# Kernel optimization log

Measured on AMD Instinct MI355X. Metric: run time of the kernel, lower is better.

## Reference

```python
import jax, jax.numpy as jnp
import numpy as np

HID = 128          # hidden_dim
IN_DIM = 256       # input_dim
BOT = 128          # bottleneck_dim
OUT = 4            # output_dim
NQ = 131072        # num query (mesh) points
E = 262144         # num grid->query edges
SEQ = 262144       # grid points (64^3)
B = 1
PE_DIM = 4 * HID   # 512, sincos embed dim over ndim=4


def _linear_params(key, fin, fout):
    k1, k2 = jax.random.split(key)
    lim = 1.0 / np.sqrt(fin)
    w = jax.random.uniform(k1, (fin, fout), minval=-lim, maxval=lim, dtype=jnp.float32)
    b = jax.random.uniform(k2, (fout,), minval=-lim, maxval=lim, dtype=jnp.float32)
    return w, b


def setup_inputs() -> dict:
    key = jax.random.key(0)
    ks = jax.random.split(key, 10)
    x = jax.random.normal(ks[0], (B, SEQ, IN_DIM), dtype=jnp.float32)
    # raw positions in [0, 200) so query_pos/100 - 1 lands in [-1, 1)
    query_pos = jax.random.uniform(ks[1], (NQ, 3), dtype=jnp.float32) * 200.0
    qidx = jnp.sort(jax.random.randint(ks[2], (E,), 0, NQ))          # sorted, as segment_csr assumes
    gidx = jax.random.randint(ks[3], (E,), 0, B * SEQ)
    grid_to_query_edges = jnp.stack([qidx, gidx], axis=1)            # [E, 2] (query_idx, grid_idx)

    msg_w0, msg_b0 = _linear_params(ks[4], IN_DIM + PE_DIM, 512)
    msg_w1, msg_b1 = _linear_params(ks[5], 512, 256)
    msg_w2, msg_b2 = _linear_params(ks[6], 256, BOT)
    pred_w0, pred_b0 = _linear_params(ks[7], BOT, 256)
    pred_w1, pred_b1 = _linear_params(ks[8], 256, OUT)
    return dict(x=x, query_pos=query_pos, grid_to_query_edges=grid_to_query_edges,
                msg_w0=msg_w0, msg_b0=msg_b0, msg_w1=msg_w1, msg_b1=msg_b1,
                msg_w2=msg_w2, msg_b2=msg_b2,
                pred_w0=pred_w0, pred_b0=pred_b0, pred_w1=pred_w1, pred_b1=pred_b1)


def _sincos_embed(coords):
    # coords: [N, 4]; dim=512 -> 128 per coord -> 64 frequencies (no padding needed)
    eff = PE_DIM // 4
    omega = 1.0 / (10000.0 ** (jnp.arange(0, eff, 2, dtype=jnp.float32) / eff))  # [64]
    out = coords[..., None] * omega                                  # [N, 4, 64]
    emb = jnp.concatenate([jnp.sin(out), jnp.cos(out)], axis=-1)     # [N, 4, 128]
    return emb.reshape(coords.shape[0], -1)                          # [N, 512]


def _gelu(x):
    return jax.nn.gelu(x, approximate=False)  # torch nn.GELU default is exact erf


def reference(x, query_pos, grid_to_query_edges,
              msg_w0, msg_b0, msg_w1, msg_b1, msg_w2, msg_b2,
              pred_w0, pred_b0, pred_w1, pred_b1):
    qp = query_pos / 100.0 - 1.0
    ones = jnp.ones((qp.shape[0], 1), dtype=qp.dtype)
    qp = jnp.concatenate([qp, ones], axis=1)                         # [NQ, 4]
    pe = _sincos_embed(qp)                                           # [NQ, 512]

    xf = x.reshape(-1, x.shape[-1])                                  # [B*SEQ, IN_DIM]
    qidx = grid_to_query_edges[:, 0]
    gidx = grid_to_query_edges[:, 1]

    feat = jnp.concatenate([xf[gidx], pe[qidx]], axis=1)             # [E, 768]
    h = _gelu(feat @ msg_w0 + msg_b0)
    h = _gelu(h @ msg_w1 + msg_b1)
    h = h @ msg_w2 + msg_b2                                          # [E, BOT]

    nq = qp.shape[0]
    sums = jax.ops.segment_sum(h, qidx, num_segments=nq)             # [NQ, BOT]
    counts = jax.ops.segment_sum(jnp.ones((h.shape[0],), h.dtype), qidx, num_segments=nq)
    mean = sums / jnp.maximum(counts, 1.0)[:, None]                  # empty segments -> 0 (segment_csr mean)

    out = _gelu(mean @ pred_w0 + pred_b0) @ pred_w1 + pred_b1        # [NQ, OUT]
    return out
```

## Files before the change

### kernel.cpp

```cpp
#include <hip/hip_runtime.h>
#include <cmath>

#define IN_DIM   256
#define H0_DIM   512
#define H1_DIM   256
#define BOT      128
#define NQ_      131072
#define NE_      262144
#define SEQ_     262144
#define QWIN     32768
#define NWIN     (NQ_/QWIN)
#define PE_K     384

static const size_t OFF_XH    = 0;
static const size_t OFF_XL    = 134217728;
static const size_t OFF_Z     = 268435456;
static const size_t OFF_PEH   = 536870912;
static const size_t OFF_PEL   = 562036736;
static const size_t OFF_H2    = 738197504;
static const size_t OFF_W0AH  = 872415232;
static const size_t OFF_W0AL  = 872677376;
static const size_t OFF_W0BH  = 872939520;
static const size_t OFF_W0BL  = 873332736;
static const size_t OFF_W1H   = 873725952;
static const size_t OFF_W1L   = 873988096;
static const size_t OFF_W2H   = 874250240;
static const size_t OFF_W2L   = 874315776;
static const size_t OFF_PW0H  = 874381312;
static const size_t OFF_PW0L  = 874446848;
static const size_t OFF_BCONST= 874512384;
static const size_t OFF_START = 874514432;
static const size_t OFF_MEANH = 0;
static const size_t OFF_MEANL = 33554432;
static const size_t OFF_G1    = 268435456;

typedef __attribute__((ext_vector_type(8))) short bf16x8;
typedef __attribute__((ext_vector_type(4))) float f32x4;

__device__ __forceinline__ float gelu_f(float v) {
    return v * 0.5f * (1.0f + erff(v * 0.7071067811865476f));
}
__device__ __forceinline__ unsigned short f2bf(float f) {
    unsigned int u = __float_as_uint(f);
    unsigned int r = (u + 0x7FFFu + ((u >> 16) & 1u)) >> 16;
    return (unsigned short)r;
}
__device__ __forceinline__ float bf2f(unsigned short h) {
    return __uint_as_float(((unsigned int)h) << 16);
}
__device__ __forceinline__ unsigned int pack2(unsigned short a, unsigned short b) {
    return (unsigned int)a | ((unsigned int)b << 16);
}
__device__ __forceinline__ void stage16(const void* g, void* l) {
    __builtin_amdgcn_global_load_lds(
        (const __attribute__((address_space(1))) unsigned int*)g,
        (__attribute__((address_space(3))) unsigned int*)l,
        16, 0, 0);
}
#define WAITV0 asm volatile("s_waitcnt vmcnt(0)" ::: "memory")
#define WAITV6 asm volatile("s_waitcnt vmcnt(6)" ::: "memory")
#define WAITV8 asm volatile("s_waitcnt vmcnt(8)" ::: "memory")
#define WAITL0 asm volatile("s_waitcnt lgkmcnt(0)" ::: "memory")

__device__ __forceinline__ void cvt4(const float4 v, unsigned int* hw, unsigned int* lw) {
    const unsigned short a = f2bf(v.x), b = f2bf(v.y), c = f2bf(v.z), d = f2bf(v.w);
    hw[0] = pack2(a, b); hw[1] = pack2(c, d);
    lw[0] = pack2(f2bf(v.x - bf2f(a)), f2bf(v.y - bf2f(b)));
    lw[1] = pack2(f2bf(v.z - bf2f(c)), f2bf(v.w - bf2f(d)));
}

__global__ __launch_bounds__(256) void conv_x(
    const float* __restrict__ x,
    unsigned short* __restrict__ xH, unsigned short* __restrict__ xL)
{
    const int wv = threadIdx.x >> 6;
    const int l  = threadIdx.x & 63;
    const int row = blockIdx.x * 4 + wv;
    const size_t base = (size_t)row * IN_DIM + l * 4;
    float4 v = *(const float4*)&x[base];
    unsigned short h0 = f2bf(v.x), h1 = f2bf(v.y), h2 = f2bf(v.z), h3 = f2bf(v.w);
    uint2 H, L;
    H.x = pack2(h0, h1); H.y = pack2(h2, h3);
    L.x = pack2(f2bf(v.x - bf2f(h0)), f2bf(v.y - bf2f(h1)));
    L.y = pack2(f2bf(v.z - bf2f(h2)), f2bf(v.w - bf2f(h3)));
    *(uint2*)&xH[base] = H;
    *(uint2*)&xL[base] = L;
}

__global__ __launch_bounds__(256) void conv_w(
    const float* __restrict__ W, unsigned short* __restrict__ WTh,
    unsigned short* __restrict__ WTl, int K, int N)
{
    int idx = blockIdx.x * 256 + threadIdx.x;
    if (idx >= K * N) return;
    int k = idx / N, n = idx % N;
    float v = W[idx];
    unsigned short h = f2bf(v);
    WTh[(size_t)n * K + k] = h;
    WTl[(size_t)n * K + k] = f2bf(v - bf2f(h));
}

__global__ __launch_bounds__(256) void bias_fold(
    const float* __restrict__ w0, const float* __restrict__ b0,
    float* __restrict__ bconst)
{
    int n = blockIdx.x * 256 + threadIdx.x;
    if (n >= H0_DIM) return;
    float s = b0[n];
    for (int j = 0; j < 64; ++j) {
        float om = exp2f((float)j * (-13.287712379549449f / 64.0f));
        s += sinf(om) * w0[(size_t)(640 + j) * H0_DIM + n];
        s += cosf(om) * w0[(size_t)(704 + j) * H0_DIM + n];
    }
    bconst[n] = s;
}

__global__ __launch_bounds__(256) void seg_offsets(
    const int* __restrict__ edges, int* __restrict__ start)
{
    int e = blockIdx.x * 256 + threadIdx.x;
    if (e > NE_) return;
    int qc = (e < NE_) ? edges[2 * e] : NQ_;
    int qp = (e > 0) ? edges[2 * e - 2] : -1;
    for (int q = qp + 1; q <= qc; ++q) start[q] = e;
}

__global__ __launch_bounds__(256) void build_pe(
    const float* __restrict__ qpos, int qbase,
    unsigned short* __restrict__ peH, unsigned short* __restrict__ peL)
{
    const int wv = threadIdx.x >> 6;
    const int l  = threadIdx.x & 63;
    const int i  = blockIdx.x * 4 + wv;
    const int i0 = l * 8;
    if (i0 >= PE_K) return;
    const int q  = qbase + i;
    const size_t base = (size_t)i * PE_K;

    const int cc = i0 >> 7;
    const int j0 = i0 & 127;
    const float cv = qpos[q * 3 + cc] * 0.01f - 1.0f;
    const bool is_sin = (j0 < 64);
    const int jj0 = j0 & 63;
    unsigned int hw[4], lw[4];
    #pragma unroll
    for (int p2 = 0; p2 < 4; ++p2) {
        unsigned short hh[2], ll[2];
        #pragma unroll
        for (int s = 0; s < 2; ++s) {
            int jj = jj0 + p2 * 2 + s;
            float om  = exp2f((float)jj * (-13.287712379549449f / 64.0f));
            float arg = cv * om;
            float v   = is_sin ? __sinf(arg) : __cosf(arg);
            unsigned short h = f2bf(v);
            hh[s] = h; ll[s] = f2bf(v - bf2f(h));
        }
        hw[p2] = pack2(hh[0], hh[1]);
        lw[p2] = pack2(ll[0], ll[1]);
    }
    uint4 H, L;
    H.x = hw[0]; H.y = hw[1]; H.z = hw[2]; H.w = hw[3];
    L.x = lw[0]; L.y = lw[1]; L.z = lw[2]; L.w = lw[3];
    *(uint4*)&peH[base + i0] = H;
    *(uint4*)&peL[base + i0] = L;
}

template <int ACT, int OUT_MODE, int GATHER>
__global__ __launch_bounds__(256) void gemm_mfma(
    const unsigned short* __restrict__ Ah, const unsigned short* __restrict__ Al,
    const unsigned short* __restrict__ Bh, const unsigned short* __restrict__ Bl,
    const float* __restrict__ bias,
    float* __restrict__ Cf, unsigned short* __restrict__ ChO, unsigned short* __restrict__ ClO,
    int M, int K, int N,
    const int* __restrict__ gp, const float* __restrict__ Zw)
{
    __shared__ __align__(16) short lds[2][4][128][32];

    const int tid = threadIdx.x;
    const int w   = tid >> 6;
    const int l   = tid & 63;
    const int l16 = l & 15;
    const int lq  = l >> 4;
    const int bm  = blockIdx.y * 128;
    const int bn  = blockIdx.x * 128;
    const int wm  = (w & 1) * 64;
    const int wn  = (w >> 1) * 64;

    f32x4 acc[4][4];
    #pragma unroll
    for (int i = 0; i < 4; ++i)
        #pragma unroll
        for (int j = 0; j < 4; ++j)
            acc[i][j] = (f32x4){0.f, 0.f, 0.f, 0.f};

    const int jrow = l >> 2;
    const int jkc  = l & 3;
    const int jswz = (jkc ^ (jrow & 3)) * 8;
    const int rswz = (lq ^ (l16 & 3)) * 8;
    const int t0 = w * 2, t1 = t0 + 1;
    const int r0 = t0 * 16 + jrow, r1 = t1 * 16 + jrow;

    size_t arow0, arow1;
    if (GATHER) {
        arow0 = (size_t)gp[2 * (bm + r0) + 1] * K;
        arow1 = (size_t)gp[2 * (bm + r1) + 1] * K;
    } else {
        arow0 = (size_t)(bm + r0) * K;
        arow1 = (size_t)(bm + r1) * K;
    }
    const size_t brow0 = (size_t)(bn + r0) * K;
    const size_t brow1 = (size_t)(bn + r1) * K;

    const int NK = K >> 5;

    auto stage_set = [&](int k, int cb) {
        const int ko = (k << 5) + jswz;
        short* base = &lds[cb][0][0][0];
        stage16(Ah + arow0 + ko, base + t0 * 512);
        stage16(Al + arow0 + ko, base + 4096 + t0 * 512);
        stage16(Bh + brow0 + ko, base + 8192 + t0 * 512);
        stage16(Bl + brow0 + ko, base + 12288 + t0 * 512);
        stage16(Ah + arow1 + ko, base + t1 * 512);
        stage16(Al + arow1 + ko, base + 4096 + t1 * 512);
        stage16(Bh + brow1 + ko, base + 8192 + t1 * 512);
        stage16(Bl + brow1 + ko, base + 12288 + t1 * 512);
    };

    stage_set(0, 0);
    if (NK > 1) stage_set(1, 1);

    for (int ks = 0; ks < NK; ++ks) {
        const int cur = ks & 1;
        if (ks == NK - 1) { WAITV0; } else { WAITV8; }
        __builtin_amdgcn_s_barrier();

        bf16x8 ah[4], al[4], bh[4], bl[4];
        #pragma unroll
        for (int i = 0; i < 4; ++i) {
            ah[i] = *(const bf16x8*)&lds[cur][0][wm + i*16 + l16][rswz];
            al[i] = *(const bf16x8*)&lds[cur][1][wm + i*16 + l16][rswz];
            bh[i] = *(const bf16x8*)&lds[cur][2][wn + i*16 + l16][rswz];
            bl[i] = *(const bf16x8*)&lds[cur][3][wn + i*16 + l16][rswz];
        }
        WAITL0;
        __builtin_amdgcn_sched_barrier(0);
        __builtin_amdgcn_s_barrier();
        if (ks + 2 < NK) stage_set(ks + 2, cur);

        #pragma unroll
        for (int i = 0; i < 4; ++i)
            #pragma unroll
            for (int j = 0; j < 4; ++j) {
                acc[i][j] = __builtin_amdgcn_mfma_f32_16x16x32_bf16(ah[i], bh[j], acc[i][j], 0, 0, 0);
                acc[i][j] = __builtin_amdgcn_mfma_f32_16x16x32_bf16(ah[i], bl[j], acc[i][j], 0, 0, 0);
                acc[i][j] = __builtin_amdgcn_mfma_f32_16x16x32_bf16(al[i], bh[j], acc[i][j], 0, 0, 0);
            }
    }

    if (OUT_MODE == 0) {
        #pragma unroll
        for (int j = 0; j < 4; ++j) {
            int n = bn + wn + j * 16 + l16;
            float bv = bias[n];
            #pragma unroll
            for (int i = 0; i < 4; ++i) {
                int mrow = bm + wm + i * 16 + lq * 4;
                #pragma unroll
                for (int r = 0; r < 4; ++r) {
                    float v = acc[i][j][r] + bv;
                    if (ACT) v = gelu_f(v);
                    Cf[(size_t)(mrow + r) * N + n] = v;
                }
            }
        }
    }
}

__global__ __launch_bounds__(256, 2) void fused_edge(
    const unsigned short* __restrict__ xHg, const unsigned short* __restrict__ xLg,
    const unsigned short* __restrict__ w0aHg, const unsigned short* __restrict__ w0aLg,
    const unsigned short* __restrict__ w1Hg, const unsigned short* __restrict__ w1Lg,
    const unsigned short* __restrict__ w2Hg, const unsigned short* __restrict__ w2Lg,
    const float* __restrict__ Zg, const float* __restrict__ b1g,
    const float* __restrict__ b2g, const int* __restrict__ gp,
    float* __restrict__ h2g)
{
    extern __shared__ __align__(16) short smem[];
    short* h0h = smem + 24576;
    short* h0l = smem + 32768;

    const int tid = threadIdx.x;
    const int w   = tid >> 6;
    const int l   = tid & 63;
    const int l16 = l & 15;
    const int lq  = l >> 4;
    const int bm  = blockIdx.x * 64;

    const int wn_p = w * 32;
    const int wn1  = w * 64;

    const int rx = tid >> 2;
    const int ux = tid & 3;
    const int sx = (ux ^ (rx & 3)) * 8;
    const int rswz = (lq ^ (l16 & 3)) * 8;
    const size_t xoff = (size_t)gp[2 * (bm + rx) + 1] * IN_DIM + sx;
    const int q_e = gp[2 * (bm + l)];
    float* lbuf = ((float*)smem) + w * 2048;

    f32x4 h1acc[4][4];
    #pragma unroll
    for (int i = 0; i < 4; ++i)
        #pragma unroll
        for (int j = 0; j < 4; ++j)
            h1acc[i][j] = (f32x4){0.f, 0.f, 0.f, 0.f};

    for (int c = 0; c < 4; ++c) {
        f32x4 acc1[4][2];
        #pragma unroll
        for (int i = 0; i < 4; ++i)
            #pragma unroll
            for (int j = 0; j < 2; ++j)
                acc1[i][j] = (f32x4){0.f, 0.f, 0.f, 0.f};

        auto stage1 = [&](int k, short* B) {
            const int ko = k << 5;
            const size_t wo = (size_t)(c * 128 + rx) * IN_DIM + ko + sx;
            stage16(xHg + xoff + ko, B + tid * 8);
            stage16(xLg + xoff + ko, B + 2048 + tid * 8);
            stage16(w0aHg + wo,                       B + 4096 + tid * 8);
            stage16(w0aHg + wo + (size_t)64 * IN_DIM, B + 6144 + tid * 8);
            stage16(w0aLg + wo,                       B + 8192 + tid * 8);
            stage16(w0aLg + wo + (size_t)64 * IN_DIM, B + 10240 + tid * 8);
        };

        stage1(0, smem);
        stage1(1, smem + 12288);
        for (int ks = 0; ks < 8; ++ks) {
            short* B = (ks & 1) ? (smem + 12288) : smem;
            if (ks == 7) { WAITV0; } else { WAITV6; }
            __builtin_amdgcn_s_barrier();

            bf16x8 ah[4], al[4], bh[2], bl[2];
            #pragma unroll
            for (int i = 0; i < 4; ++i) {
                const int ro = (i * 16 + l16) * 32 + rswz;
                ah[i] = *(const bf16x8*)&B[ro];
                al[i] = *(const bf16x8*)&B[2048 + ro];
            }
            #pragma unroll
            for (int j = 0; j < 2; ++j) {
                const int ro = (wn_p + j * 16 + l16) * 32 + rswz;
                bh[j] = *(const bf16x8*)&B[4096 + ro];
                bl[j] = *(const bf16x8*)&B[8192 + ro];
            }
            WAITL0;
            __builtin_amdgcn_sched_barrier(0);
            __builtin_amdgcn_s_barrier();
            if (ks < 6) stage1(ks + 2, B);

            #pragma unroll
            for (int i = 0; i < 4; ++i)
                #pragma unroll
                for (int j = 0; j < 2; ++j) {
                    acc1[i][j] = __builtin_amdgcn_mfma_f32_16x16x32_bf16(ah[i], bh[j], acc1[i][j], 0, 0, 0);
                    acc1[i][j] = __builtin_amdgcn_mfma_f32_16x16x32_bf16(ah[i], bl[j], acc1[i][j], 0, 0, 0);
                    acc1[i][j] = __builtin_amdgcn_mfma_f32_16x16x32_bf16(al[i], bh[j], acc1[i][j], 0, 0, 0);
                }
        }
        __syncthreads();

        #pragma unroll
        for (int j = 0; j < 2; ++j)
            #pragma unroll
            for (int i = 0; i < 4; ++i)
                #pragma unroll
                for (int r = 0; r < 4; ++r) {
                    const int rowq = i * 16 + lq * 4 + r;
                    const int u = j * 4 + (l16 >> 2);
                    lbuf[rowq * 32 + (((u ^ (rowq & 7)) << 2) | (l16 & 3))] = acc1[i][j][r];
                }
        __syncthreads();
        {
            const float* zrow = Zg + (size_t)q_e * H0_DIM + c * 128 + wn_p;
            #pragma unroll
            for (int g = 0; g < 2; ++g) {
                unsigned int hw[8], lw[8];
                #pragma unroll
                for (int c2 = 0; c2 < 4; ++c2) {
                    const int cq = g * 4 + c2;
                    float4 v = *(const float4*)&lbuf[l * 32 + ((cq ^ (l & 7)) << 2)];
                    const float4 z = *(const float4*)&zrow[cq * 4];
                    v.x = gelu_f(v.x + z.x); v.y = gelu_f(v.y + z.y);
                    v.z = gelu_f(v.z + z.z); v.w = gelu_f(v.w + z.w);
                    cvt4(v, &hw[c2 * 2], &lw[c2 * 2]);
                }
                const int u0 = (wn_p >> 3) + g * 2;
                const int o0 = l * 128 + (((u0    ) ^ (l & 7)) << 3);
                const int o1 = l * 128 + (((u0 + 1) ^ (l & 7)) << 3);
                uint4 H0, H1, L0, L1;
                H0.x = hw[0]; H0.y = hw[1]; H0.z = hw[2]; H0.w = hw[3];
                H1.x = hw[4]; H1.y = hw[5]; H1.z = hw[6]; H1.w = hw[7];
                L0.x = lw[0]; L0.y = lw[1]; L0.z = lw[2]; L0.w = lw[3];
                L1.x = lw[4]; L1.y = lw[5]; L1.z = lw[6]; L1.w = lw[7];
                *(uint4*)&h0h[o0] = H0; *(uint4*)&h0h[o1] = H1;
                *(uint4*)&h0l[o0] = L0; *(uint4*)&h0l[o1] = L1;
            }
        }
        __syncthreads();

        {
            #pragma unroll
            for (int p = 0; p < 4; ++p) {
                const size_t o = (size_t)(rx + 64 * p) * H0_DIM + c * 128 + sx;
                stage16(w1Hg + o, smem + p * 2048 + tid * 8);
                stage16(w1Lg + o, smem + 8192 + p * 2048 + tid * 8);
            }
        }
        __syncthreads();
        for (int ks = 0; ks < 4; ++ks) {
            bf16x8 ah[4], al[4], bh[4], bl[4];
            #pragma unroll
            for (int i = 0; i < 4; ++i) {
                const int row = i * 16 + l16;
                const int uo = ((ks * 4 + lq) ^ (row & 7)) << 3;
                ah[i] = *(const bf16x8*)&h0h[row * 128 + uo];
                al[i] = *(const bf16x8*)&h0l[row * 128 + uo];
            }
            #pragma unroll
            for (int j = 0; j < 4; ++j) {
                const int ro = (wn1 + j * 16 + l16) * 32 + rswz;
                bh[j] = *(const bf16x8*)&smem[ro];
                bl[j] = *(const bf16x8*)&smem[8192 + ro];
            }
            __syncthreads();
            if (ks < 3) {
                #pragma unroll
                for (int p = 0; p < 4; ++p) {
                    const size_t o = (size_t)(rx + 64 * p) * H0_DIM + c * 128 + (ks + 1) * 32 + sx;
                    stage16(w1Hg + o, smem + p * 2048 + tid * 8);
                    stage16(w1Lg + o, smem + 8192 + p * 2048 + tid * 8);
                }
            }
            #pragma unroll
            for (int i = 0; i < 4; ++i)
                #pragma unroll
                for (int j = 0; j < 4; ++j) {
                    h1acc[i][j] = __builtin_amdgcn_mfma_f32_16x16x32_bf16(ah[i], bh[j], h1acc[i][j], 0, 0, 0);
                    h1acc[i][j] = __builtin_amdgcn_mfma_f32_16x16x32_bf16(ah[i], bl[j], h1acc[i][j], 0, 0, 0);
                    h1acc[i][j] = __builtin_amdgcn_mfma_f32_16x16x32_bf16(al[i], bh[j], h1acc[i][j], 0, 0, 0);
                }
            __syncthreads();
        }
    }

    f32x4 acc2[4][2];
    #pragma unroll
    for (int i = 0; i < 4; ++i)
        #pragma unroll
        for (int j = 0; j < 2; ++j)
            acc2[i][j] = (f32x4){0.f, 0.f, 0.f, 0.f};

    for (int kh = 0; kh < 2; ++kh) {
        const bool my = ((w >> 1) == kh);
        #pragma unroll
        for (int j2 = 0; j2 < 2; ++j2) {
            if (my) {
                #pragma unroll
                for (int jj = 0; jj < 2; ++jj) {
                    const int j = j2 * 2 + jj;
                    const float bv = b1g[wn1 + j * 16 + l16];
                    #pragma unroll
                    for (int i = 0; i < 4; ++i)
                        #pragma unroll
                        for (int r = 0; r < 4; ++r) {
                            const int rowq = i * 16 + lq * 4 + r;
                            const int u = jj * 4 + (l16 >> 2);
                            lbuf[rowq * 32 + (((u ^ (rowq & 7)) << 2) | (l16 & 3))] =
                                gelu_f(h1acc[i][j][r] + bv);
                        }
                }
            }
            __syncthreads();
            if (my) {
                const int colb = (w & 1) * 64 + j2 * 32;
                #pragma unroll
                for (int g = 0; g < 2; ++g) {
                    unsigned int hw[8], lw[8];
                    #pragma unroll
                    for (int c2 = 0; c2 < 4; ++c2) {
                        const int cq = g * 4 + c2;
                        float4 v = *(const float4*)&lbuf[l * 32 + ((cq ^ (l & 7)) << 2)];
                        cvt4(v, &hw[c2 * 2], &lw[c2 * 2]);
                    }
                    const int u0 = ((colb + g * 16) >> 3);
                    const int o0 = l * 128 + (((u0    ) ^ (l & 7)) << 3);
                    const int o1 = l * 128 + (((u0 + 1) ^ (l & 7)) << 3);
                    uint4 H0, H1, L0, L1;
                    H0.x = hw[0]; H0.y = hw[1]; H0.z = hw[2]; H0.w = hw[3];
                    H1.x = hw[4]; H1.y = hw[5]; H1.z = hw[6]; H1.w = hw[7];
                    L0.x = lw[0]; L0.y = lw[1]; L0.z = lw[2]; L0.w = lw[3];
                    L1.x = lw[4]; L1.y = lw[5]; L1.z = lw[6]; L1.w = lw[7];
                    *(uint4*)&h0h[o0] = H0; *(uint4*)&h0h[o1] = H1;
                    *(uint4*)&h0l[o0] = L0; *(uint4*)&h0l[o1] = L1;
                }
            }
            __syncthreads();
        }

        {
            #pragma unroll
            for (int p = 0; p < 2; ++p) {
                const size_t o = (size_t)(rx + 64 * p) * H1_DIM + kh * 128 + sx;
                stage16(w2Hg + o, smem + p * 2048 + tid * 8);
                stage16(w2Lg + o, smem + 4096 + p * 2048 + tid * 8);
            }
        }
        __syncthreads();
        for (int ks = 0; ks < 4; ++ks) {
            bf16x8 ah[4], al[4], bh[2], bl[2];
            #pragma unroll
            for (int i = 0; i < 4; ++i) {
                const int row = i * 16 + l16;
                const int uo = ((ks * 4 + lq) ^ (row & 7)) << 3;
                ah[i] = *(const bf16x8*)&h0h[row * 128 + uo];
                al[i] = *(const bf16x8*)&h0l[row * 128 + uo];
            }
            #pragma unroll
            for (int j = 0; j < 2; ++j) {
                const int ro = (wn_p + j * 16 + l16) * 32 + rswz;
                bh[j] = *(const bf16x8*)&smem[ro];
                bl[j] = *(const bf16x8*)&smem[4096 + ro];
            }
            __syncthreads();
            if (ks < 3) {
                #pragma unroll
                for (int p = 0; p < 2; ++p) {
                    const size_t o = (size_t)(rx + 64 * p) * H1_DIM + kh * 128 + (ks + 1) * 32 + sx;
                    stage16(w2Hg + o, smem + p * 2048 + tid * 8);
                    stage16(w2Lg + o, smem + 4096 + p * 2048 + tid * 8);
                }
            }
            #pragma unroll
            for (int i = 0; i < 4; ++i)
                #pragma unroll
                for (int j = 0; j < 2; ++j) {
                    acc2[i][j] = __builtin_amdgcn_mfma_f32_16x16x32_bf16(ah[i], bh[j], acc2[i][j], 0, 0, 0);
                    acc2[i][j] = __builtin_amdgcn_mfma_f32_16x16x32_bf16(ah[i], bl[j], acc2[i][j], 0, 0, 0);
                    acc2[i][j] = __builtin_amdgcn_mfma_f32_16x16x32_bf16(al[i], bh[j], acc2[i][j], 0, 0, 0);
                }
            __syncthreads();
        }
    }

    #pragma unroll
    for (int j = 0; j < 2; ++j) {
        const int n = wn_p + j * 16 + l16;
        const float bv = b2g[n];
        #pragma unroll
        for (int i = 0; i < 4; ++i) {
            const int er = bm + i * 16 + lq * 4;
            #pragma unroll
            for (int r = 0; r < 4; ++r)
                h2g[(size_t)(er + r) * BOT + n] = acc2[i][j][r] + bv;
        }
    }
}

__global__ __launch_bounds__(256) void seg_mean(
    const int* __restrict__ start, const float* __restrict__ h2,
    unsigned short* __restrict__ mH, unsigned short* __restrict__ mL)
{
    const int t = threadIdx.x;
    const int q = blockIdx.x * 8 + (t >> 5);
    const int quad = t & 31;
    const int s = start[q];
    const int e = start[q + 1];

    float4 acc = make_float4(0.f, 0.f, 0.f, 0.f);
    for (int i = s; i < e; ++i) {
        const float4 v = *(const float4*)&h2[(size_t)i * BOT + quad * 4];
        acc.x += v.x; acc.y += v.y; acc.z += v.z; acc.w += v.w;
    }
    const float inv = 1.0f / (float)((e - s) > 0 ? (e - s) : 1);
    float m0 = acc.x * inv, m1 = acc.y * inv, m2 = acc.z * inv, m3 = acc.w * inv;
    unsigned short h0 = f2bf(m0), h1 = f2bf(m1), h2s = f2bf(m2), h3 = f2bf(m3);
    uint2 H, L;
    H.x = pack2(h0, h1); H.y = pack2(h2s, h3);
    L.x = pack2(f2bf(m0 - bf2f(h0)), f2bf(m1 - bf2f(h1)));
    L.y = pack2(f2bf(m2 - bf2f(h2s)), f2bf(m3 - bf2f(h3)));
    *(uint2*)&mH[(size_t)q * BOT + quad * 4] = H;
    *(uint2*)&mL[(size_t)q * BOT + quad * 4] = L;
}

__global__ __launch_bounds__(256) void pred1_kernel(
    const float* __restrict__ g1, const float* __restrict__ w,
    const float* __restrict__ b, float* __restrict__ out)
{
    const int wave = threadIdx.x >> 6;
    const int lane = threadIdx.x & 63;
    const int row  = blockIdx.x * 4 + wave;

    const float* g = g1 + (size_t)row * 256;
    float a0 = 0, a1 = 0, a2 = 0, a3 = 0;
    #pragma unroll
    for (int i = 0; i < 4; ++i) {
        int k = lane + 64 * i;
        float gv = g[k];
        const float* wr = w + k * 4;
        a0 = fmaf(gv, wr[0], a0);
        a1 = fmaf(gv, wr[1], a1);
        a2 = fmaf(gv, wr[2], a2);
        a3 = fmaf(gv, wr[3], a3);
    }
    #pragma unroll
    for (int off = 32; off > 0; off >>= 1) {
        a0 += __shfl_down(a0, off, 64);
        a1 += __shfl_down(a1, off, 64);
        a2 += __shfl_down(a2, off, 64);
        a3 += __shfl_down(a3, off, 64);
    }
    if (lane == 0) {
        float4 o = {a0 + b[0], a1 + b[1], a2 + b[2], a3 + b[3]};
        *(float4*)&out[(size_t)row * 4] = o;
    }
}

extern "C" void kernel_launch(void* const* d_in, const int* in_sizes, int n_in,
                              void* d_out, int out_size, void* d_ws, size_t ws_size,
                              hipStream_t stream)
{
    const float* x    = (const float*)d_in[0];
    const float* qpos = (const float*)d_in[1];
    const int*   edges= (const int*)  d_in[2];
    const float* w0   = (const float*)d_in[3];
    const float* b0   = (const float*)d_in[4];
    const float* w1   = (const float*)d_in[5];
    const float* b1   = (const float*)d_in[6];
    const float* w2   = (const float*)d_in[7];
    const float* b2   = (const float*)d_in[8];
    const float* pw0  = (const float*)d_in[9];
    const float* pb0  = (const float*)d_in[10];
    const float* pw1  = (const float*)d_in[11];
    const float* pb1  = (const float*)d_in[12];
    float* out = (float*)d_out;

    char* ws = (char*)d_ws;
    unsigned short* xH    = (unsigned short*)(ws + OFF_XH);
    unsigned short* xL    = (unsigned short*)(ws + OFF_XL);
    float*          Z     = (float*)(ws + OFF_Z);
    unsigned short* peH   = (unsigned short*)(ws + OFF_PEH);
    unsigned short* peL   = (unsigned short*)(ws + OFF_PEL);
    float*          h2    = (float*)(ws + OFF_H2);
    unsigned short* w0aH  = (unsigned short*)(ws + OFF_W0AH);
    unsigned short* w0aL  = (unsigned short*)(ws + OFF_W0AL);
    unsigned short* w0bH  = (unsigned short*)(ws + OFF_W0BH);
    unsigned short* w0bL  = (unsigned short*)(ws + OFF_W0BL);
    unsigned short* w1H   = (unsigned short*)(ws + OFF_W1H);
    unsigned short* w1L   = (unsigned short*)(ws + OFF_W1L);
    unsigned short* w2H   = (unsigned short*)(ws + OFF_W2H);
    unsigned short* w2L   = (unsigned short*)(ws + OFF_W2L);
    unsigned short* pw0H  = (unsigned short*)(ws + OFF_PW0H);
    unsigned short* pw0L  = (unsigned short*)(ws + OFF_PW0L);
    float*          bconst= (float*)(ws + OFF_BCONST);
    int*            start = (int*)(ws + OFF_START);
    unsigned short* meanH = (unsigned short*)(ws + OFF_MEANH);
    unsigned short* meanL = (unsigned short*)(ws + OFF_MEANL);
    float*          g1    = (float*)(ws + OFF_G1);

    static bool attr_done = false;
    if (!attr_done) {
        hipFuncSetAttribute(reinterpret_cast<const void*>(&fused_edge),
                            hipFuncAttributeMaxDynamicSharedMemorySize, 81920);
        attr_done = true;
    }

    conv_x<<<SEQ_/4, 256, 0, stream>>>(x, xH, xL);
    conv_w<<<(IN_DIM*H0_DIM + 255)/256, 256, 0, stream>>>(w0, w0aH, w0aL, IN_DIM, H0_DIM);
    conv_w<<<(PE_K*H0_DIM + 255)/256, 256, 0, stream>>>(w0 + (size_t)IN_DIM*H0_DIM, w0bH, w0bL, PE_K, H0_DIM);
    conv_w<<<(H0_DIM*H1_DIM + 255)/256, 256, 0, stream>>>(w1, w1H, w1L, H0_DIM, H1_DIM);
    conv_w<<<(H1_DIM*BOT + 255)/256, 256, 0, stream>>>(w2, w2H, w2L, H1_DIM, BOT);
    conv_w<<<(BOT*H1_DIM + 255)/256, 256, 0, stream>>>(pw0, pw0H, pw0L, BOT, H1_DIM);
    bias_fold<<<2, 256, 0, stream>>>(w0, b0, bconst);
    seg_offsets<<<(NE_ + 1 + 255)/256, 256, 0, stream>>>(edges, start);

    for (int wn = 0; wn < NWIN; ++wn) {
        build_pe<<<QWIN/4, 256, 0, stream>>>(qpos, wn * QWIN, peH, peL);
        gemm_mfma<0, 0, 0><<<dim3(H0_DIM/128, QWIN/128), 256, 0, stream>>>(
            peH, peL, w0bH, w0bL, bconst, Z + (size_t)wn * QWIN * H0_DIM,
            nullptr, nullptr, QWIN, PE_K, H0_DIM, nullptr, nullptr);
    }

    fused_edge<<<NE_/64, 256, 81920, stream>>>(
        xH, xL, w0aH, w0aL, w1H, w1L, w2H, w2L,
        Z, b1, b2, edges, h2);

    seg_mean<<<NQ_/8, 256, 0, stream>>>(start, h2, meanH, meanL);
    gemm_mfma<1, 0, 0><<<dim3(H1_DIM/128, NQ_/128), 256, 0, stream>>>(
        meanH, meanL, pw0H, pw0L, pb0, g1, nullptr, nullptr,
        NQ_, BOT, H1_DIM, nullptr, nullptr);
    pred1_kernel<<<NQ_/4, 256, 0, stream>>>(g1, pw1, pb1, out);
}
```

Measured before the change: 1.850 ms.

## Load weight fragments directly from global memory, staging only activations in LDS

The GEMM and fused edge kernels now read weight (B) fragments straight from global memory into registers, relying on cache, and stage only the gathered activation rows into LDS. The fused edge kernel is restructured around this: the first layer runs in two halves of 256 columns with a triple-buffered x stage, and the layer-1/layer-2 hand-offs use smaller per-wave scratch buffers. The explicit vmcnt waits are replaced by __syncthreads, and the generic GEMM gets a 3-blocks-per-CU launch bound. This cuts LDS traffic and LDS footprint per block, at the cost of repeated uncoalesced global reads of weights and coarser synchronisation.

```diff
diff --git a/kernel.cpp b/kernel.cpp
--- a/kernel.cpp
+++ b/kernel.cpp
@@ -57,11 +57,6 @@
         (__attribute__((address_space(3))) unsigned int*)l,
         16, 0, 0);
 }
-#define WAITV0 asm volatile("s_waitcnt vmcnt(0)" ::: "memory")
-#define WAITV6 asm volatile("s_waitcnt vmcnt(6)" ::: "memory")
-#define WAITV8 asm volatile("s_waitcnt vmcnt(8)" ::: "memory")
-#define WAITL0 asm volatile("s_waitcnt lgkmcnt(0)" ::: "memory")
-
 __device__ __forceinline__ void cvt4(const float4 v, unsigned int* hw, unsigned int* lw) {
     const unsigned short a = f2bf(v.x), b = f2bf(v.y), c = f2bf(v.z), d = f2bf(v.w);
     hw[0] = pack2(a, b); hw[1] = pack2(c, d);
@@ -165,16 +160,14 @@
     *(uint4*)&peL[base + i0] = L;
 }
 
-template <int ACT, int OUT_MODE, int GATHER>
-__global__ __launch_bounds__(256) void gemm_mfma(
+template <int ACT>
+__global__ __launch_bounds__(256, 3) void gemm_mfma(
     const unsigned short* __restrict__ Ah, const unsigned short* __restrict__ Al,
     const unsigned short* __restrict__ Bh, const unsigned short* __restrict__ Bl,
-    const float* __restrict__ bias,
-    float* __restrict__ Cf, unsigned short* __restrict__ ChO, unsigned short* __restrict__ ClO,
-    int M, int K, int N,
-    const int* __restrict__ gp, const float* __restrict__ Zw)
-{
-    __shared__ __align__(16) short lds[2][4][128][32];
+    const float* __restrict__ bias, float* __restrict__ Cf,
+    int M, int K, int N)
+{
+    __shared__ __align__(16) short lds[2][2][128][32];
 
     const int tid = threadIdx.x;
     const int w   = tid >> 6;
@@ -193,84 +186,76 @@
         for (int j = 0; j < 4; ++j)
             acc[i][j] = (f32x4){0.f, 0.f, 0.f, 0.f};
 
-    const int jrow = l >> 2;
-    const int jkc  = l & 3;
-    const int jswz = (jkc ^ (jrow & 3)) * 8;
-    const int rswz = (lq ^ (l16 & 3)) * 8;
-    const int t0 = w * 2, t1 = t0 + 1;
-    const int r0 = t0 * 16 + jrow, r1 = t1 * 16 + jrow;
-
-    size_t arow0, arow1;
-    if (GATHER) {
-        arow0 = (size_t)gp[2 * (bm + r0) + 1] * K;
-        arow1 = (size_t)gp[2 * (bm + r1) + 1] * K;
-    } else {
-        arow0 = (size_t)(bm + r0) * K;
-        arow1 = (size_t)(bm + r1) * K;
-    }
-    const size_t brow0 = (size_t)(bn + r0) * K;
-    const size_t brow1 = (size_t)(bn + r1) * K;
+    const int swu = ((l & 3) ^ ((l >> 3) & 3)) * 8;
+    size_t asrc[2];
+    #pragma unroll
+    for (int p = 0; p < 2; ++p) {
+        const int row = p * 64 + w * 16 + (l >> 2);
+        asrc[p] = (size_t)(bm + row) * K + swu;
+    }
+    unsigned int bidx[4];
+    #pragma unroll
+    for (int j = 0; j < 4; ++j)
+        bidx[j] = (unsigned)(bn + wn + j * 16 + l16) * (unsigned)K + lq * 8;
 
     const int NK = K >> 5;
 
-    auto stage_set = [&](int k, int cb) {
-        const int ko = (k << 5) + jswz;
+    auto stg = [&](int k, int cb) {
+        const int ko = k << 5;
         short* base = &lds[cb][0][0][0];
-        stage16(Ah + arow0 + ko, base + t0 * 512);
-        stage16(Al + arow0 + ko, base + 4096 + t0 * 512);
-        stage16(Bh + brow0 + ko, base + 8192 + t0 * 512);
-        stage16(Bl + brow0 + ko, base + 12288 + t0 * 512);
-        stage16(Ah + arow1 + ko, base + t1 * 512);
-        stage16(Al + arow1 + ko, base + 4096 + t1 * 512);
-        stage16(Bh + brow1 + ko, base + 8192 + t1 * 512);
-        stage16(Bl + brow1 + ko, base + 12288 + t1 * 512);
+        #pragma unroll
+        for (int p = 0; p < 2; ++p) {
+            stage16(Ah + asrc[p] + ko, base + (p * 256 + w * 64) * 8);
+            stage16(Al + asrc[p] + ko, base + 4096 + (p * 256 + w * 64) * 8);
+        }
     };
 
-    stage_set(0, 0);
-    if (NK > 1) stage_set(1, 1);
-
+    stg(0, 0);
+    if (NK > 1) stg(1, 1);
+
+    const int rs = (l16 >> 1) & 3;
     for (int ks = 0; ks < NK; ++ks) {
-        const int cur = ks & 1;
-        if (ks == NK - 1) { WAITV0; } else { WAITV8; }
-        __builtin_amdgcn_s_barrier();
-
-        bf16x8 ah[4], al[4], bh[4], bl[4];
+        const int cb = ks & 1;
+        const int ko = ks << 5;
+        __syncthreads();
+
+        bf16x8 a_h[4], a_l[4], b_h[4], b_l[4];
         #pragma unroll
         for (int i = 0; i < 4; ++i) {
-            ah[i] = *(const bf16x8*)&lds[cur][0][wm + i*16 + l16][rswz];
-            al[i] = *(const bf16x8*)&lds[cur][1][wm + i*16 + l16][rswz];
-            bh[i] = *(const bf16x8*)&lds[cur][2][wn + i*16 + l16][rswz];
-            bl[i] = *(const bf16x8*)&lds[cur][3][wn + i*16 + l16][rswz];
-        }
-        WAITL0;
-        __builtin_amdgcn_sched_barrier(0);
-        __builtin_amdgcn_s_barrier();
-        if (ks + 2 < NK) stage_set(ks + 2, cur);
-
+            const int row = wm + i * 16 + l16;
+            const int so  = (lq ^ rs) * 8;
+            a_h[i] = *(const bf16x8*)&lds[cb][0][row][so];
+            a_l[i] = *(const bf16x8*)&lds[cb][1][row][so];
+        }
+        #pragma unroll
+        for (int j = 0; j < 4; ++j) {
+            b_h[j] = *(const bf16x8*)&Bh[bidx[j] + ko];
+            b_l[j] = *(const bf16x8*)&Bl[bidx[j] + ko];
+        }
         #pragma unroll
         for (int i = 0; i < 4; ++i)
             #pragma unroll
             for (int j = 0; j < 4; ++j) {
-                acc[i][j] = __builtin_amdgcn_mfma_f32_16x16x32_bf16(ah[i], bh[j], acc[i][j], 0, 0, 0);
-                acc[i][j] = __builtin_amdgcn_mfma_f32_16x16x32_bf16(ah[i], bl[j], acc[i][j], 0, 0, 0);
-                acc[i][j] = __builtin_amdgcn_mfma_f32_16x16x32_bf16(al[i], bh[j], acc[i][j], 0, 0, 0);
-            }
-    }
-
-    if (OUT_MODE == 0) {
-        #pragma unroll
-        for (int j = 0; j < 4; ++j) {
-            int n = bn + wn + j * 16 + l16;
-            float bv = bias[n];
-            #pragma unroll
-            for (int i = 0; i < 4; ++i) {
-                int mrow = bm + wm + i * 16 + lq * 4;
-                #pragma unroll
-                for (int r = 0; r < 4; ++r) {
-                    float v = acc[i][j][r] + bv;
-                    if (ACT) v = gelu_f(v);
-                    Cf[(size_t)(mrow + r) * N + n] = v;
-                }
+                acc[i][j] = __builtin_amdgcn_mfma_f32_16x16x32_bf16(a_h[i], b_h[j], acc[i][j], 0, 0, 0);
+                acc[i][j] = __builtin_amdgcn_mfma_f32_16x16x32_bf16(a_h[i], b_l[j], acc[i][j], 0, 0, 0);
+                acc[i][j] = __builtin_amdgcn_mfma_f32_16x16x32_bf16(a_l[i], b_h[j], acc[i][j], 0, 0, 0);
+            }
+        __syncthreads();
+        if (ks + 2 < NK) stg(ks + 2, cb);
+    }
+
+    #pragma unroll
+    for (int j = 0; j < 4; ++j) {
+        int n = bn + wn + j * 16 + l16;
+        float bv = bias[n];
+        #pragma unroll
+        for (int i = 0; i < 4; ++i) {
+            int mrow = bm + wm + i * 16 + lq * 4;
+            #pragma unroll
+            for (int r = 0; r < 4; ++r) {
+                float v = acc[i][j][r] + bv;
+                if (ACT) v = gelu_f(v);
+                Cf[(size_t)(mrow + r) * N + n] = v;
             }
         }
     }
@@ -296,16 +281,26 @@
     const int lq  = l >> 4;
     const int bm  = blockIdx.x * 64;
 
-    const int wn_p = w * 32;
-    const int wn1  = w * 64;
-
-    const int rx = tid >> 2;
-    const int ux = tid & 3;
-    const int sx = (ux ^ (rx & 3)) * 8;
-    const int rswz = (lq ^ (l16 & 3)) * 8;
-    const size_t xoff = (size_t)gp[2 * (bm + rx) + 1] * IN_DIM + sx;
+    const int rA = w * 8 + (l >> 3);
+    const int gidxA = gp[2 * (bm + rA) + 1];
+    const int gidxB = gp[2 * (bm + rA + 32) + 1];
+    const int swu = ((l & 7) ^ ((l >> 3) & 7)) * 8;
+    const unsigned int xoA = (unsigned)gidxA * 256u + swu;
+    const unsigned int xoB = (unsigned)gidxB * 256u + swu;
     const int q_e = gp[2 * (bm + l)];
-    float* lbuf = ((float*)smem) + w * 2048;
+
+    unsigned int w0idx[4], w1idx[4], w2idx[2];
+    #pragma unroll
+    for (int j = 0; j < 4; ++j) {
+        const unsigned n = (unsigned)((j >> 1) * 128 + w * 32 + (j & 1) * 16 + l16);
+        w0idx[j] = n * 256u + lq * 8;
+        w1idx[j] = n * 512u + lq * 8;
+    }
+    #pragma unroll
+    for (int j = 0; j < 2; ++j)
+        w2idx[j] = (unsigned)(w * 32 + j * 16 + l16) * 256u + lq * 8;
+
+    const unsigned int zq = (unsigned)q_e * 512u;
 
     f32x4 h1acc[4][4];
     #pragma unroll
@@ -314,89 +309,90 @@
         for (int j = 0; j < 4; ++j)
             h1acc[i][j] = (f32x4){0.f, 0.f, 0.f, 0.f};
 
-    for (int c = 0; c < 4; ++c) {
-        f32x4 acc1[4][2];
+    auto stageA = [&](int ck, int slot) {
+        short* T = smem + slot * 8192;
+        const int ko = ck << 6;
+        stage16(xHg + xoA + ko, T + w * 512);
+        stage16(xHg + xoB + ko, T + 2048 + w * 512);
+        stage16(xLg + xoA + ko, T + 4096 + w * 512);
+        stage16(xLg + xoB + ko, T + 6144 + w * 512);
+    };
+
+    stageA(0, 0);
+    stageA(1, 1);
+
+    const int rsw7 = l16 & 7;
+
+    for (int half = 0; half < 2; ++half) {
+        f32x4 acc1[4][4];
         #pragma unroll
         for (int i = 0; i < 4; ++i)
             #pragma unroll
-            for (int j = 0; j < 2; ++j)
+            for (int j = 0; j < 4; ++j)
                 acc1[i][j] = (f32x4){0.f, 0.f, 0.f, 0.f};
 
-        auto stage1 = [&](int k, short* B) {
-            const int ko = k << 5;
-            const size_t wo = (size_t)(c * 128 + rx) * IN_DIM + ko + sx;
-            stage16(xHg + xoff + ko, B + tid * 8);
-            stage16(xLg + xoff + ko, B + 2048 + tid * 8);
-            stage16(w0aHg + wo,                       B + 4096 + tid * 8);
-            stage16(w0aHg + wo + (size_t)64 * IN_DIM, B + 6144 + tid * 8);
-            stage16(w0aLg + wo,                       B + 8192 + tid * 8);
-            stage16(w0aLg + wo + (size_t)64 * IN_DIM, B + 10240 + tid * 8);
-        };
-
-        stage1(0, smem);
-        stage1(1, smem + 12288);
-        for (int ks = 0; ks < 8; ++ks) {
-            short* B = (ks & 1) ? (smem + 12288) : smem;
-            if (ks == 7) { WAITV0; } else { WAITV6; }
-            __builtin_amdgcn_s_barrier();
-
-            bf16x8 ah[4], al[4], bh[2], bl[2];
-            #pragma unroll
-            for (int i = 0; i < 4; ++i) {
-                const int ro = (i * 16 + l16) * 32 + rswz;
-                ah[i] = *(const bf16x8*)&B[ro];
-                al[i] = *(const bf16x8*)&B[2048 + ro];
-            }
-            #pragma unroll
-            for (int j = 0; j < 2; ++j) {
-                const int ro = (wn_p + j * 16 + l16) * 32 + rswz;
-                bh[j] = *(const bf16x8*)&B[4096 + ro];
-                bl[j] = *(const bf16x8*)&B[8192 + ro];
-            }
-            WAITL0;
-            __builtin_amdgcn_sched_barrier(0);
-            __builtin_amdgcn_s_barrier();
-            if (ks < 6) stage1(ks + 2, B);
-
-            #pragma unroll
-            for (int i = 0; i < 4; ++i)
-                #pragma unroll
-                for (int j = 0; j < 2; ++j) {
-                    acc1[i][j] = __builtin_amdgcn_mfma_f32_16x16x32_bf16(ah[i], bh[j], acc1[i][j], 0, 0, 0);
-                    acc1[i][j] = __builtin_amdgcn_mfma_f32_16x16x32_bf16(ah[i], bl[j], acc1[i][j], 0, 0, 0);
-                    acc1[i][j] = __builtin_amdgcn_mfma_f32_16x16x32_bf16(al[i], bh[j], acc1[i][j], 0, 0, 0);
+        const unsigned hof = (unsigned)half * 65536u;
+
+        for (int ks = 0; ks < 4; ++ks) {
+            const int t = half * 4 + ks;
+            short* T = smem + (t % 3) * 8192;
+            __syncthreads();
+            if (t + 2 < 8) stageA((t + 2) & 3, (t + 2) % 3);
+
+            #pragma unroll
+            for (int q = 0; q < 2; ++q) {
+                bf16x8 a_h[4], a_l[4], b_h[4], b_l[4];
+                #pragma unroll
+                for (int i = 0; i < 4; ++i) {
+                    const int ro = (i * 16 + l16) * 64 + (((q * 4 + lq) ^ rsw7) << 3);
+                    a_h[i] = *(const bf16x8*)&T[ro];
+                    a_l[i] = *(const bf16x8*)&T[4096 + ro];
                 }
-        }
-        __syncthreads();
-
-        #pragma unroll
-        for (int j = 0; j < 2; ++j)
-            #pragma unroll
-            for (int i = 0; i < 4; ++i)
-                #pragma unroll
-                for (int r = 0; r < 4; ++r) {
-                    const int rowq = i * 16 + lq * 4 + r;
-                    const int u = j * 4 + (l16 >> 2);
-                    lbuf[rowq * 32 + (((u ^ (rowq & 7)) << 2) | (l16 & 3))] = acc1[i][j][r];
+                const unsigned ko2 = hof + (unsigned)(ks * 64 + q * 32);
+                #pragma unroll
+                for (int j = 0; j < 4; ++j) {
+                    b_h[j] = *(const bf16x8*)&w0aHg[w0idx[j] + ko2];
+                    b_l[j] = *(const bf16x8*)&w0aLg[w0idx[j] + ko2];
                 }
-        __syncthreads();
-        {
-            const float* zrow = Zg + (size_t)q_e * H0_DIM + c * 128 + wn_p;
-            #pragma unroll
-            for (int g = 0; g < 2; ++g) {
+                #pragma unroll
+                for (int i = 0; i < 4; ++i)
+                    #pragma unroll
+                    for (int j = 0; j < 4; ++j) {
+                        acc1[i][j] = __builtin_amdgcn_mfma_f32_16x16x32_bf16(a_h[i], b_h[j], acc1[i][j], 0, 0, 0);
+                        acc1[i][j] = __builtin_amdgcn_mfma_f32_16x16x32_bf16(a_h[i], b_l[j], acc1[i][j], 0, 0, 0);
+                        acc1[i][j] = __builtin_amdgcn_mfma_f32_16x16x32_bf16(a_l[i], b_h[j], acc1[i][j], 0, 0, 0);
+                    }
+            }
+        }
+
+        float* lbuf = (float*)(smem + ((half * 4 + 3) % 3) * 8192) + w * 1024;
+
+        for (int sub = 0; sub < 2; ++sub) {
+            __syncthreads();
+            #pragma unroll
+            for (int jj = 0; jj < 2; ++jj) {
+                const int j = sub * 2 + jj;
+                #pragma unroll
+                for (int i = 0; i < 4; ++i)
+                    #pragma unroll
+                    for (int r = 0; r < 4; ++r) {
+                        const int rowq = i * 16 + lq * 4 + r;
+                        const int u = l16 >> 2;
+                        lbuf[rowq * 16 + (((u ^ ((rowq >> 1) & 3)) << 2) | (l16 & 3))] = acc1[i][j][r];
+                    }
+                const unsigned zc = zq + (unsigned)(half * 256 + sub * 128 + w * 32 + jj * 16);
                 unsigned int hw[8], lw[8];
                 #pragma unroll
-                for (int c2 = 0; c2 < 4; ++c2) {
-                    const int cq = g * 4 + c2;
-                    float4 v = *(const float4*)&lbuf[l * 32 + ((cq ^ (l & 7)) << 2)];
-                    const float4 z = *(const float4*)&zrow[cq * 4];
+                for (int i4 = 0; i4 < 4; ++i4) {
+                    float4 v = *(const float4*)&lbuf[l * 16 + ((i4 ^ ((l >> 1) & 3)) << 2)];
+                    const float4 z = *(const float4*)&Zg[zc + i4 * 4];
                     v.x = gelu_f(v.x + z.x); v.y = gelu_f(v.y + z.y);
                     v.z = gelu_f(v.z + z.z); v.w = gelu_f(v.w + z.w);
-                    cvt4(v, &hw[c2 * 2], &lw[c2 * 2]);
+                    cvt4(v, &hw[i4 * 2], &lw[i4 * 2]);
                 }
-                const int u0 = (wn_p >> 3) + g * 2;
-                const int o0 = l * 128 + (((u0    ) ^ (l & 7)) << 3);
-                const int o1 = l * 128 + (((u0 + 1) ^ (l & 7)) << 3);
+                const int cu0 = w * 4 + jj * 2;
+                const int o0 = l * 128 + (((cu0    ) ^ (l & 7)) << 3);
+                const int o1 = l * 128 + (((cu0 + 1) ^ (l & 7)) << 3);
                 uint4 H0, H1, L0, L1;
                 H0.x = hw[0]; H0.y = hw[1]; H0.z = hw[2]; H0.w = hw[3];
                 H1.x = hw[4]; H1.y = hw[5]; H1.z = hw[6]; H1.w = hw[7];
@@ -405,51 +401,33 @@
                 *(uint4*)&h0h[o0] = H0; *(uint4*)&h0h[o1] = H1;
                 *(uint4*)&h0l[o0] = L0; *(uint4*)&h0l[o1] = L1;
             }
-        }
-        __syncthreads();
-
-        {
-            #pragma unroll
-            for (int p = 0; p < 4; ++p) {
-                const size_t o = (size_t)(rx + 64 * p) * H0_DIM + c * 128 + sx;
-                stage16(w1Hg + o, smem + p * 2048 + tid * 8);
-                stage16(w1Lg + o, smem + 8192 + p * 2048 + tid * 8);
-            }
-        }
-        __syncthreads();
-        for (int ks = 0; ks < 4; ++ks) {
-            bf16x8 ah[4], al[4], bh[4], bl[4];
-            #pragma unroll
-            for (int i = 0; i < 4; ++i) {
-                const int row = i * 16 + l16;
-                const int uo = ((ks * 4 + lq) ^ (row & 7)) << 3;
-                ah[i] = *(const bf16x8*)&h0h[row * 128 + uo];
-                al[i] = *(const bf16x8*)&h0l[row * 128 + uo];
-            }
-            #pragma unroll
-            for (int j = 0; j < 4; ++j) {
-                const int ro = (wn1 + j * 16 + l16) * 32 + rswz;
-                bh[j] = *(const bf16x8*)&smem[ro];
-                bl[j] = *(const bf16x8*)&smem[8192 + ro];
-            }
             __syncthreads();
-            if (ks < 3) {
-                #pragma unroll
-                for (int p = 0; p < 4; ++p) {
-                    const size_t o = (size_t)(rx + 64 * p) * H0_DIM + c * 128 + (ks + 1) * 32 + sx;
-                    stage16(w1Hg + o, smem + p * 2048 + tid * 8);
-                    stage16(w1Lg + o, smem + 8192 + p * 2048 + tid * 8);
+
+            const unsigned kbase = (unsigned)(half * 256 + sub * 128);
+            #pragma unroll
+            for (int ks2 = 0; ks2 < 4; ++ks2) {
+                bf16x8 a_h[4], a_l[4], b_h[4], b_l[4];
+                #pragma unroll
+                for (int i = 0; i < 4; ++i) {
+                    const int ro = (i * 16 + l16) * 128 + (((ks2 * 4 + lq) ^ rsw7) << 3);
+                    a_h[i] = *(const bf16x8*)&h0h[ro];
+                    a_l[i] = *(const bf16x8*)&h0l[ro];
                 }
-            }
-            #pragma unroll
-            for (int i = 0; i < 4; ++i)
+                const unsigned ko2 = kbase + ks2 * 32;
                 #pragma unroll
                 for (int j = 0; j < 4; ++j) {
-                    h1acc[i][j] = __builtin_amdgcn_mfma_f32_16x16x32_bf16(ah[i], bh[j], h1acc[i][j], 0, 0, 0);
-                    h1acc[i][j] = __builtin_amdgcn_mfma_f32_16x16x32_bf16(ah[i], bl[j], h1acc[i][j], 0, 0, 0);
-                    h1acc[i][j] = __builtin_amdgcn_mfma_f32_16x16x32_bf16(al[i], bh[j], h1acc[i][j], 0, 0, 0);
+                    b_h[j] = *(const bf16x8*)&w1Hg[w1idx[j] + ko2];
+                    b_l[j] = *(const bf16x8*)&w1Lg[w1idx[j] + ko2];
                 }
-            __syncthreads();
+                #pragma unroll
+                for (int i = 0; i < 4; ++i)
+                    #pragma unroll
+                    for (int j = 0; j < 4; ++j) {
+                        h1acc[i][j] = __builtin_amdgcn_mfma_f32_16x16x32_bf16(a_h[i], b_h[j], h1acc[i][j], 0, 0, 0);
+                        h1acc[i][j] = __builtin_amdgcn_mfma_f32_16x16x32_bf16(a_h[i], b_l[j], h1acc[i][j], 0, 0, 0);
+                        h1acc[i][j] = __builtin_amdgcn_mfma_f32_16x16x32_bf16(a_l[i], b_h[j], h1acc[i][j], 0, 0, 0);
+                    }
+            }
         }
     }
 
@@ -460,101 +438,71 @@
         for (int j = 0; j < 2; ++j)
             acc2[i][j] = (f32x4){0.f, 0.f, 0.f, 0.f};
 
+    float* lbuf2 = (float*)smem + w * 1024;
+
     for (int kh = 0; kh < 2; ++kh) {
-        const bool my = ((w >> 1) == kh);
-        #pragma unroll
-        for (int j2 = 0; j2 < 2; ++j2) {
-            if (my) {
-                #pragma unroll
-                for (int jj = 0; jj < 2; ++jj) {
-                    const int j = j2 * 2 + jj;
-                    const float bv = b1g[wn1 + j * 16 + l16];
-                    #pragma unroll
-                    for (int i = 0; i < 4; ++i)
-                        #pragma unroll
-                        for (int r = 0; r < 4; ++r) {
-                            const int rowq = i * 16 + lq * 4 + r;
-                            const int u = jj * 4 + (l16 >> 2);
-                            lbuf[rowq * 32 + (((u ^ (rowq & 7)) << 2) | (l16 & 3))] =
-                                gelu_f(h1acc[i][j][r] + bv);
-                        }
+        __syncthreads();
+        #pragma unroll
+        for (int jj = 0; jj < 2; ++jj) {
+            const int j = kh * 2 + jj;
+            const float bv = b1g[kh * 128 + w * 32 + jj * 16 + l16];
+            #pragma unroll
+            for (int i = 0; i < 4; ++i)
+                #pragma unroll
+                for (int r = 0; r < 4; ++r) {
+                    const int rowq = i * 16 + lq * 4 + r;
+                    const int u = l16 >> 2;
+                    lbuf2[rowq * 16 + (((u ^ ((rowq >> 1) & 3)) << 2) | (l16 & 3))] =
+                        gelu_f(h1acc[i][j][r] + bv);
                 }
-            }
-            __syncthreads();
-            if (my) {
-                const int colb = (w & 1) * 64 + j2 * 32;
-                #pragma unroll
-                for (int g = 0; g < 2; ++g) {
-                    unsigned int hw[8], lw[8];
-                    #pragma unroll
-                    for (int c2 = 0; c2 < 4; ++c2) {
-                        const int cq = g * 4 + c2;
-                        float4 v = *(const float4*)&lbuf[l * 32 + ((cq ^ (l & 7)) << 2)];
-                        cvt4(v, &hw[c2 * 2], &lw[c2 * 2]);
-                    }
-                    const int u0 = ((colb + g * 16) >> 3);
-                    const int o0 = l * 128 + (((u0    ) ^ (l & 7)) << 3);
-                    const int o1 = l * 128 + (((u0 + 1) ^ (l & 7)) << 3);
-                    uint4 H0, H1, L0, L1;
-                    H0.x = hw[0]; H0.y = hw[1]; H0.z = hw[2]; H0.w = hw[3];
-                    H1.x = hw[4]; H1.y = hw[5]; H1.z = hw[6]; H1.w = hw[7];
-                    L0.x = lw[0]; L0.y = lw[1]; L0.z = lw[2]; L0.w = lw[3];
-                    L1.x = lw[4]; L1.y = lw[5]; L1.z = lw[6]; L1.w = lw[7];
-                    *(uint4*)&h0h[o0] = H0; *(uint4*)&h0h[o1] = H1;
-                    *(uint4*)&h0l[o0] = L0; *(uint4*)&h0l[o1] = L1;
+            unsigned int hw[8], lw[8];
+            #pragma unroll
+            for (int i4 = 0; i4 < 4; ++i4) {
+                float4 v = *(const float4*)&lbuf2[l * 16 + ((i4 ^ ((l >> 1) & 3)) << 2)];
+                cvt4(v, &hw[i4 * 2], &lw[i4 * 2]);
+            }
+            const int cu0 = w * 4 + jj * 2;
+            const int o0 = l * 128 + (((cu0    ) ^ (l & 7)) << 3);
+            const int o1 = l * 128 + (((cu0 + 1) ^ (l & 7)) << 3);
+            uint4 H0, H1, L0, L1;
+            H0.x = hw[0]; H0.y = hw[1]; H0.z = hw[2]; H0.w = hw[3];
+            H1.x = hw[4]; H1.y = hw[5]; H1.z = hw[6]; H1.w = hw[7];
+            L0.x = lw[0]; L0.y = lw[1]; L0.z = lw[2]; L0.w = lw[3];
+            L1.x = lw[4]; L1.y = lw[5]; L1.z = lw[6]; L1.w = lw[7];
+            *(uint4*)&h0h[o0] = H0; *(uint4*)&h0h[o1] = H1;
+            *(uint4*)&h0l[o0] = L0; *(uint4*)&h0l[o1] = L1;
+        }
+        __syncthreads();
+
+        #pragma unroll
+        for (int ks2 = 0; ks2 < 4; ++ks2) {
+            bf16x8 a_h[4], a_l[4], b_h[2], b_l[2];
+            #pragma unroll
+            for (int i = 0; i < 4; ++i) {
+                const int ro = (i * 16 + l16) * 128 + (((ks2 * 4 + lq) ^ rsw7) << 3);
+                a_h[i] = *(const bf16x8*)&h0h[ro];
+                a_l[i] = *(const bf16x8*)&h0l[ro];
+            }
+            const unsigned ko2 = (unsigned)(kh * 128 + ks2 * 32);
+            #pragma unroll
+            for (int j = 0; j < 2; ++j) {
+                b_h[j] = *(const bf16x8*)&w2Hg[w2idx[j] + ko2];
+                b_l[j] = *(const bf16x8*)&w2Lg[w2idx[j] + ko2];
+            }
+            #pragma unroll
+            for (int i = 0; i < 4; ++i)
+                #pragma unroll
+                for (int j = 0; j < 2; ++j) {
+                    acc2[i][j] = __builtin_amdgcn_mfma_f32_16x16x32_bf16(a_h[i], b_h[j], acc2[i][j], 0, 0, 0);
+                    acc2[i][j] = __builtin_amdgcn_mfma_f32_16x16x32_bf16(a_h[i], b_l[j], acc2[i][j], 0, 0, 0);
+                    acc2[i][j] = __builtin_amdgcn_mfma_f32_16x16x32_bf16(a_l[i], b_h[j], acc2[i][j], 0, 0, 0);
                 }
-            }
-            __syncthreads();
-        }
-
-        {
-            #pragma unroll
-            for (int p = 0; p < 2; ++p) {
-                const size_t o = (size_t)(rx + 64 * p) * H1_DIM + kh * 128 + sx;
-                stage16(w2Hg + o, smem + p * 2048 + tid * 8);
-                stage16(w2Lg + o, smem + 4096 + p * 2048 + tid * 8);
-            }
-        }
-        __syncthreads();
-        for (int ks = 0; ks < 4; ++ks) {
-            bf16x8 ah[4], al[4], bh[2], bl[2];
-            #pragma unroll
-            for (int i = 0; i < 4; ++i) {
-                const int row = i * 16 + l16;
-                const int uo = ((ks * 4 + lq) ^ (row & 7)) << 3;
-                ah[i] = *(const bf16x8*)&h0h[row * 128 + uo];
-                al[i] = *(const bf16x8*)&h0l[row * 128 + uo];
-            }
-            #pragma unroll
-            for (int j = 0; j < 2; ++j) {
-                const int ro = (wn_p + j * 16 + l16) * 32 + rswz;
-                bh[j] = *(const bf16x8*)&smem[ro];
-                bl[j] = *(const bf16x8*)&smem[4096 + ro];
-            }
-            __syncthreads();
-            if (ks < 3) {
-                #pragma unroll
-                for (int p = 0; p < 2; ++p) {
-                    const size_t o = (size_t)(rx + 64 * p) * H1_DIM + kh * 128 + (ks + 1) * 32 + sx;
-                    stage16(w2Hg + o, smem + p * 2048 + tid * 8);
-                    stage16(w2Lg + o, smem + 4096 + p * 2048 + tid * 8);
-                }
-            }
-            #pragma unroll
-            for (int i = 0; i < 4; ++i)
-                #pragma unroll
-                for (int j = 0; j < 2; ++j) {
-                    acc2[i][j] = __builtin_amdgcn_mfma_f32_16x16x32_bf16(ah[i], bh[j], acc2[i][j], 0, 0, 0);
-                    acc2[i][j] = __builtin_amdgcn_mfma_f32_16x16x32_bf16(ah[i], bl[j], acc2[i][j], 0, 0, 0);
-                    acc2[i][j] = __builtin_amdgcn_mfma_f32_16x16x32_bf16(al[i], bh[j], acc2[i][j], 0, 0, 0);
-                }
-            __syncthreads();
         }
     }
 
     #pragma unroll
     for (int j = 0; j < 2; ++j) {
-        const int n = wn_p + j * 16 + l16;
+        const int n = w * 32 + j * 16 + l16;
         const float bv = b2g[n];
         #pragma unroll
         for (int i = 0; i < 4; ++i) {
@@ -685,9 +633,9 @@
 
     for (int wn = 0; wn < NWIN; ++wn) {
         build_pe<<<QWIN/4, 256, 0, stream>>>(qpos, wn * QWIN, peH, peL);
-        gemm_mfma<0, 0, 0><<<dim3(H0_DIM/128, QWIN/128), 256, 0, stream>>>(
+        gemm_mfma<0><<<dim3(H0_DIM/128, QWIN/128), 256, 0, stream>>>(
             peH, peL, w0bH, w0bL, bconst, Z + (size_t)wn * QWIN * H0_DIM,
-            nullptr, nullptr, QWIN, PE_K, H0_DIM, nullptr, nullptr);
+            QWIN, PE_K, H0_DIM);
     }
 
     fused_edge<<<NE_/64, 256, 81920, stream>>>(
@@ -695,8 +643,7 @@
         Z, b1, b2, edges, h2);
 
     seg_mean<<<NQ_/8, 256, 0, stream>>>(start, h2, meanH, meanL);
-    gemm_mfma<1, 0, 0><<<dim3(H1_DIM/128, NQ_/128), 256, 0, stream>>>(
-        meanH, meanL, pw0H, pw0L, pb0, g1, nullptr, nullptr,
-        NQ_, BOT, H1_DIM, nullptr, nullptr);
+    gemm_mfma<1><<<dim3(H1_DIM/128, NQ_/128), 256, 0, stream>>>(
+        meanH, meanL, pw0H, pw0L, pb0, g1, NQ_, BOT, H1_DIM);
     pred1_kernel<<<NQ_/4, 256, 0, stream>>>(g1, pw1, pb1, out);
 }
```

After: 2.575 ms. 39.2% more time.
